# Performance work log

Measured on AMD Instinct MI355X. Metric: run time of the kernel, lower is better.

The kernel has to match this reference:

```python
import jax, jax.numpy as jnp
import numpy as np

B, T, D_MODEL, D_HEAD = 8, 2048, 1024, 64


def setup_inputs() -> dict:
    key = jax.random.key(0)
    kx, kq, kk, kv = jax.random.split(key, 4)
    s = 1.0 / np.sqrt(D_MODEL)
    return {
        "x": jax.random.normal(kx, (B, T, D_MODEL), dtype=jnp.float32),
        "W_Q": jax.random.normal(kq, (D_MODEL, D_HEAD), dtype=jnp.float32) * s,
        "W_K": jax.random.normal(kk, (D_MODEL, D_HEAD), dtype=jnp.float32) * s,
        "W_V": jax.random.normal(kv, (D_MODEL, D_HEAD), dtype=jnp.float32) * s,
    }


def reference(x, W_Q, W_K, W_V):
    # x: [B, T, d_model]; projections -> [B, T, d_head]
    q = jnp.einsum("btd,dh->bth", x, W_Q)
    k = jnp.einsum("btd,dh->bth", x, W_K)
    v = jnp.einsum("btd,dh->bth", x, W_V)
    d_head = W_Q.shape[-1]
    scale = 1.0 / jnp.sqrt(jnp.asarray(d_head, dtype=x.dtype))
    # scores: [B, T, T], causal mask (lower-triangular kept)
    scores = jnp.einsum("bqh,bkh->bqk", q, k) * scale
    T_ = x.shape[1]
    causal = jnp.tril(jnp.ones((T_, T_), dtype=bool))
    scores = jnp.where(causal[None, :, :], scores, jnp.asarray(-jnp.inf, dtype=x.dtype))
    a = jax.nn.softmax(scores, axis=-1)
    # dropout omitted (eval mode / identity)
    out = jnp.einsum("bqk,bkh->bqh", a, v)
    return out
```

## Files before the change

kernel.cpp:

```cpp
#include <hip/hip_runtime.h>

#define TT   2048
#define DM   1024
#define DH   64
#define NB   8
#define BK   128
#define KST  72

typedef __attribute__((ext_vector_type(4))) float          f32x4;
typedef __attribute__((ext_vector_type(4))) int            i32x4;
typedef __attribute__((ext_vector_type(4))) unsigned short u16x4;
typedef __attribute__((ext_vector_type(8))) short          s16x8;

__device__ __forceinline__ unsigned short f2bf(float f) {
  unsigned int u = __float_as_uint(f);
  u += 0x7fffu + ((u >> 16) & 1u);
  return (unsigned short)(u >> 16);
}

#define MFMA(acc, a, b) \
  (acc) = __builtin_amdgcn_mfma_f32_16x16x32_bf16((a), (b), (acc), 0, 0, 0)

__device__ __forceinline__ void gload_lds16(const void* g, void* l) {
  __builtin_amdgcn_global_load_lds(
      (const __attribute__((address_space(1))) void*)g,
      (__attribute__((address_space(3))) void*)l, 16, 0, 0);
}

#define WS_WT    0u
#define WS_QK    393216u
#define WS_VT    4587520u
#define WS_OP    6684672u
#define WS_ML    24510464u

__global__ __launch_bounds__(256) void pack_w_kernel(
    const float* __restrict__ wq, const float* __restrict__ wk,
    const float* __restrict__ wv, unsigned short* __restrict__ wt) {
  int idx = blockIdx.x * 256 + threadIdx.x;
  if (idx >= 192 * DM) return;
  int n = idx >> 10;
  int k = idx & (DM - 1);
  const float* src = (n < 64) ? wq : ((n < 128) ? wk : wv);
  wt[(size_t)n * DM + k] = f2bf(src[(size_t)k * DH + (n & 63)]);
}

__global__ __launch_bounds__(256) void qkv_gemm_kernel(
    const float* __restrict__ x, const unsigned short* __restrict__ wt,
    unsigned short* __restrict__ qkvqk, unsigned short* __restrict__ vt) {
  __shared__ __align__(16) float          a_lds[32 * BK];
  __shared__ __align__(16) unsigned short b_lds[192 * BK];

  const int tid  = threadIdx.x;
  const int lane = tid & 63;
  const int w    = tid >> 6;
  const int ln   = lane & 15;
  const int quad = lane >> 4;
  const int mw   = w & 1;
  const int nw   = w >> 1;
  const int m0   = blockIdx.x * 32;
  const int n0   = nw * 96;
  const int lsw  = ln & 7;

  int agoff[4];
  #pragma unroll
  for (int i = 0; i < 4; ++i) {
    int s = i * 256 + w * 64 + lane;
    int m = s >> 5, cc = s & 31;
    agoff[i] = (m0 + m) * DM + ((cc ^ (m & 7)) << 2);
  }
  int bgoff[12];
  #pragma unroll
  for (int j = 0; j < 12; ++j) {
    int s = j * 256 + w * 64 + lane;
    int n = s >> 4, cc = s & 15;
    bgoff[j] = n * DM + ((cc ^ (n & 7)) << 3);
  }

  f32x4 acc[6];
  #pragma unroll
  for (int i = 0; i < 6; ++i) acc[i] = (f32x4){0.f, 0.f, 0.f, 0.f};
  union { s16x8 v; unsigned short h[8]; } ap;

  #pragma unroll
  for (int i = 0; i < 4; ++i)
    gload_lds16(x + agoff[i], (void*)(a_lds + (i * 256 + w * 64) * 4));
  #pragma unroll
  for (int j = 0; j < 12; ++j)
    gload_lds16(wt + bgoff[j], (void*)(b_lds + (j * 256 + w * 64) * 8));

  for (int k0 = 0; k0 < DM; k0 += BK) {
    __syncthreads();
    #pragma unroll
    for (int ks = 0; ks < BK; ks += 32) {
      const int m  = mw * 16 + ln;
      const int c0 = (ks >> 2) + 2 * quad;
      f32x4 v0 = *(const f32x4*)&a_lds[m * BK + ((c0 ^ lsw) << 2)];
      f32x4 v1 = *(const f32x4*)&a_lds[m * BK + (((c0 + 1) ^ lsw) << 2)];
      #pragma unroll
      for (int j = 0; j < 4; ++j) { ap.h[j] = f2bf(v0[j]); ap.h[4 + j] = f2bf(v1[j]); }
      s16x8 af = ap.v;
      const int cb = (ks >> 3) + quad;
      #pragma unroll
      for (int nt = 0; nt < 6; ++nt) {
        int n = n0 + nt * 16 + ln;
        s16x8 bf = *(const s16x8*)&b_lds[n * BK + ((cb ^ lsw) << 3)];
        MFMA(acc[nt], af, bf);
      }
    }
    __syncthreads();
    if (k0 + BK < DM) {
      const int kn = k0 + BK;
      #pragma unroll
      for (int i = 0; i < 4; ++i)
        gload_lds16(x + agoff[i] + kn, (void*)(a_lds + (i * 256 + w * 64) * 4));
      #pragma unroll
      for (int j = 0; j < 12; ++j)
        gload_lds16(wt + bgoff[j] + kn, (void*)(b_lds + (j * 256 + w * 64) * 8));
    }
  }

  const float QS = 0.18033688011112042f;
  const int mm0 = m0 + mw * 16;
  const int bz  = mm0 >> 11;
  const int tb  = (mm0 & 2047) + quad * 4;
  #pragma unroll
  for (int nt = 0; nt < 6; ++nt) {
    const int ncol = n0 + nt * 16 + ln;
    if (ncol < 128) {
      const float sc = (ncol < 64) ? QS : 1.0f;
      #pragma unroll
      for (int r = 0; r < 4; ++r) {
        int row = mm0 + quad * 4 + r;
        qkvqk[(size_t)row * 128 + ncol] = f2bf(acc[nt][r] * sc);
      }
    } else {
      int d = ncol - 128;
      u16x4 h;
      #pragma unroll
      for (int r = 0; r < 4; ++r) h[r] = f2bf(acc[nt][r]);
      *(u16x4*)(vt + ((size_t)bz * 64 + d) * TT + tb) = h;
    }
  }
}

__global__ __launch_bounds__(512) void attn_part_kernel(
    const unsigned short* __restrict__ qkvqk, const unsigned short* __restrict__ vt,
    unsigned short* __restrict__ opart, float* __restrict__ ml) {
  const int Ctab[16] = {0,1,3,6,10,15,21,28,36,45,55,66,78,91,105,120};
  const int f  = blockIdx.x;
  const int bz = f / 136;
  const int rw = f - bz * 136;
  int s = 0;
  #pragma unroll
  for (int t = 1; t < 16; ++t) if (rw >= Ctab[t]) s = t;
  const int c = rw - Ctab[s];

  __shared__ __align__(16) unsigned short k_lds[2][64 * 64];
  __shared__ __align__(16) unsigned short v_lds[2][64 * 64];
  __shared__ __align__(16) unsigned short p_lds[2 * 64 * KST];

  const int tid  = threadIdx.x;
  const int w    = tid >> 6;
  const int grp  = w >> 2;
  const int wq   = w & 3;
  const int lane = tid & 63;
  const int ln   = lane & 15;
  const int quad = lane >> 4;
  const int lsw  = ln & 7;
  const int bb   = bz * TT;
  const int kbase = c * 128;
  const int qt   = 2 * s + grp;

  const int slot = w * 64 + lane;
  const int srow = slot >> 3, scc = slot & 7;
  const unsigned short* kgp =
      qkvqk + (size_t)(bb + kbase + srow) * 128 + 64 + ((scc ^ (srow & 7)) << 3);
  const unsigned short* vgp =
      vt + ((size_t)bz * 64 + srow) * TT + kbase + ((scc ^ (srow & 7)) << 3);

  const unsigned short* qrow = qkvqk + (size_t)(bb + qt * 64 + wq * 16 + ln) * 128;
  const s16x8 qf0 = *(const s16x8*)(qrow + quad * 8);
  const s16x8 qf1 = *(const s16x8*)(qrow + 32 + quad * 8);

  s16x8 ones;
  #pragma unroll
  for (int j = 0; j < 8; ++j) ones[j] = (short)0x3F80;

  f32x4 acc_o[4], acc_l;
  #pragma unroll
  for (int i = 0; i < 4; ++i) acc_o[i] = (f32x4){0.f, 0.f, 0.f, 0.f};
  acc_l = (f32x4){0.f, 0.f, 0.f, 0.f};

  unsigned short* pb = p_lds + grp * 64 * KST;
  const int qg = qt * 64 + wq * 16 + quad * 4;

  gload_lds16(kgp, (void*)(k_lds[0] + (w * 64) * 8));
  gload_lds16(vgp, (void*)(v_lds[0] + (w * 64) * 8));
  __syncthreads();
  gload_lds16(kgp + 64 * 128, (void*)(k_lds[1] + (w * 64) * 8));
  gload_lds16(vgp + 64,       (void*)(v_lds[1] + (w * 64) * 8));

  #pragma unroll
  for (int ct = 0; ct < 2; ++ct) {
    const unsigned short* kb = k_lds[ct];
    const unsigned short* vb = v_lds[ct];
    const int ktg = c * 2 + ct;
    if (ktg <= qt) {
      const bool diag = (ktg == qt);
      f32x4 acc_s[4];
      #pragma unroll
      for (int i = 0; i < 4; ++i) acc_s[i] = (f32x4){0.f, 0.f, 0.f, 0.f};
      __builtin_amdgcn_s_setprio(1);
      #pragma unroll
      for (int ns = 0; ns < 4; ++ns) {
        const int krow = ns * 16 + ln;
        s16x8 kf0 = *(const s16x8*)&kb[krow * 64 + ((quad ^ lsw) << 3)];
        s16x8 kf1 = *(const s16x8*)&kb[krow * 64 + (((4 + quad) ^ lsw) << 3)];
        MFMA(acc_s[ns], qf0, kf0);
        MFMA(acc_s[ns], qf1, kf1);
      }
      __builtin_amdgcn_s_setprio(0);
      #pragma unroll
      for (int r = 0; r < 4; ++r) {
        const int qgr = qg + r;
        #pragma unroll
        for (int ns = 0; ns < 4; ++ns) {
          float sv = acc_s[ns][r];
          if (diag) {
            int kg = ktg * 64 + ns * 16 + ln;
            sv = (kg <= qgr) ? sv : -1e30f;
          }
          pb[(wq * 16 + quad * 4 + r) * KST + ns * 16 + ln] =
              f2bf(__builtin_amdgcn_exp2f(sv));
        }
      }
      __builtin_amdgcn_s_setprio(1);
      #pragma unroll
      for (int kk = 0; kk < 64; kk += 32) {
        s16x8 pf = *(const s16x8*)&pb[(wq * 16 + ln) * KST + kk + quad * 8];
        MFMA(acc_l, pf, ones);
        #pragma unroll
        for (int nt = 0; nt < 4; ++nt) {
          const int d  = nt * 16 + ln;
          const int sc = ((kk >> 3) + quad) ^ lsw;
          s16x8 vf = *(const s16x8*)&vb[d * 64 + sc * 8];
          MFMA(acc_o[nt], pf, vf);
        }
      }
      __builtin_amdgcn_s_setprio(0);
      asm volatile("" ::: "memory");
    }
    if (ct == 0) __syncthreads();
  }

  const int base = (qt & 1) ? (s + 1) * (s + 1) : s * (s + 1);
  const size_t slab = (size_t)bz * 272 + base + c;
  unsigned short* op = opart + slab * 4096;
  #pragma unroll
  for (int nt = 0; nt < 4; ++nt)
    #pragma unroll
    for (int r = 0; r < 4; ++r)
      op[(wq * 16 + quad * 4 + r) * 64 + nt * 16 + ln] = f2bf(acc_o[nt][r]);
  if (ln == 0) {
    float* lp = ml + slab * 64;
    #pragma unroll
    for (int r = 0; r < 4; ++r)
      lp[wq * 16 + quad * 4 + r] = acc_l[r];
  }
}

__global__ __launch_bounds__(256) void attn_combine_kernel(
    const unsigned short* __restrict__ opart, const float* __restrict__ ml,
    float* __restrict__ out) {
  const int qt = blockIdx.x;
  const int bz = blockIdx.y;
  const int g  = qt >> 1;
  const int nch = g + 1;
  const int base = (qt & 1) ? (g + 1) * (g + 1) : g * (g + 1);
  const size_t slab0 = (size_t)bz * 272 + base;

  const int tid = threadIdx.x;
  const int row = tid >> 2;
  const int ds  = (tid & 3) * 16;

  float L = 0.f;
  float acc[16];
  #pragma unroll
  for (int j = 0; j < 16; ++j) acc[j] = 0.f;
  #pragma unroll 4
  for (int ch = 0; ch < nch; ++ch) {
    L += ml[(slab0 + ch) * 64 + row];
    const unsigned short* op = opart + (slab0 + ch) * 4096 + row * 64 + ds;
    i32x4 v0 = *(const i32x4*)(op);
    i32x4 v1 = *(const i32x4*)(op + 8);
    #pragma unroll
    for (int j = 0; j < 4; ++j) {
      unsigned int u0 = (unsigned int)v0[j], u1 = (unsigned int)v1[j];
      acc[j * 2]         += __uint_as_float(u0 << 16);
      acc[j * 2 + 1]     += __uint_as_float(u0 & 0xffff0000u);
      acc[8 + j * 2]     += __uint_as_float(u1 << 16);
      acc[8 + j * 2 + 1] += __uint_as_float(u1 & 0xffff0000u);
    }
  }
  float inv = 1.0f / L;
  float* o = out + ((size_t)bz * TT + qt * 64 + row) * 64 + ds;
  #pragma unroll
  for (int j = 0; j < 16; ++j) o[j] = acc[j] * inv;
}

extern "C" void kernel_launch(void* const* d_in, const int* in_sizes, int n_in,
                              void* d_out, int out_size, void* d_ws, size_t ws_size,
                              hipStream_t stream) {
  const float* x  = (const float*)d_in[0];
  const float* wq = (const float*)d_in[1];
  const float* wk = (const float*)d_in[2];
  const float* wv = (const float*)d_in[3];
  float* out = (float*)d_out;

  char* ws = (char*)d_ws;
  unsigned short* wt    = (unsigned short*)(ws + WS_WT);
  unsigned short* qkvqk = (unsigned short*)(ws + WS_QK);
  unsigned short* vt    = (unsigned short*)(ws + WS_VT);
  unsigned short* opart = (unsigned short*)(ws + WS_OP);
  float*          ml    = (float*)(ws + WS_ML);

  pack_w_kernel<<<(192 * DM + 255) / 256, 256, 0, stream>>>(wq, wk, wv, wt);
  qkv_gemm_kernel<<<NB * TT / 32, 256, 0, stream>>>(x, wt, qkvqk, vt);
  attn_part_kernel<<<NB * 136, 512, 0, stream>>>(qkvqk, vt, opart, ml);
  attn_combine_kernel<<<dim3(32, NB), 256, 0, stream>>>(opart, ml, out);
}
```

Measured before the change: 131.2 us.

## Split attention blocks to one query tile each with swizzled P buffer

New measurement: 131.5 us. No clear change (+0.3%).

```diff
diff --git a/kernel.cpp b/kernel.cpp
--- a/kernel.cpp
+++ b/kernel.cpp
@@ -5,7 +5,6 @@
 #define DH   64
 #define NB   8
 #define BK   128
-#define KST  72
 
 typedef __attribute__((ext_vector_type(4))) float          f32x4;
 typedef __attribute__((ext_vector_type(4))) int            i32x4;
@@ -143,42 +142,37 @@
   }
 }
 
-__global__ __launch_bounds__(512) void attn_part_kernel(
+__global__ __launch_bounds__(256) void attn_part_kernel(
     const unsigned short* __restrict__ qkvqk, const unsigned short* __restrict__ vt,
     unsigned short* __restrict__ opart, float* __restrict__ ml) {
-  const int Ctab[16] = {0,1,3,6,10,15,21,28,36,45,55,66,78,91,105,120};
   const int f  = blockIdx.x;
-  const int bz = f / 136;
-  const int rw = f - bz * 136;
-  int s = 0;
-  #pragma unroll
-  for (int t = 1; t < 16; ++t) if (rw >= Ctab[t]) s = t;
-  const int c = rw - Ctab[s];
+  const int bz = f / 272;
+  const int rw = f - bz * 272;
+  int qt = 0;
+  #pragma unroll
+  for (int t = 1; t < 32; ++t) {
+    int tg = t >> 1;
+    int bs = (t & 1) ? (tg + 1) * (tg + 1) : tg * (tg + 1);
+    if (rw >= bs) qt = t;
+  }
+  const int g    = qt >> 1;
+  const int base = (qt & 1) ? (g + 1) * (g + 1) : g * (g + 1);
+  const int c    = rw - base;
 
   __shared__ __align__(16) unsigned short k_lds[2][64 * 64];
   __shared__ __align__(16) unsigned short v_lds[2][64 * 64];
-  __shared__ __align__(16) unsigned short p_lds[2 * 64 * KST];
+  __shared__ __align__(16) unsigned short p_lds[64 * 64];
 
   const int tid  = threadIdx.x;
   const int w    = tid >> 6;
-  const int grp  = w >> 2;
-  const int wq   = w & 3;
   const int lane = tid & 63;
   const int ln   = lane & 15;
   const int quad = lane >> 4;
   const int lsw  = ln & 7;
   const int bb   = bz * TT;
   const int kbase = c * 128;
-  const int qt   = 2 * s + grp;
-
-  const int slot = w * 64 + lane;
-  const int srow = slot >> 3, scc = slot & 7;
-  const unsigned short* kgp =
-      qkvqk + (size_t)(bb + kbase + srow) * 128 + 64 + ((scc ^ (srow & 7)) << 3);
-  const unsigned short* vgp =
-      vt + ((size_t)bz * 64 + srow) * TT + kbase + ((scc ^ (srow & 7)) << 3);
-
-  const unsigned short* qrow = qkvqk + (size_t)(bb + qt * 64 + wq * 16 + ln) * 128;
+
+  const unsigned short* qrow = qkvqk + (size_t)(bb + qt * 64 + w * 16 + ln) * 128;
   const s16x8 qf0 = *(const s16x8*)(qrow + quad * 8);
   const s16x8 qf1 = *(const s16x8*)(qrow + 32 + quad * 8);
 
@@ -191,14 +185,42 @@
   for (int i = 0; i < 4; ++i) acc_o[i] = (f32x4){0.f, 0.f, 0.f, 0.f};
   acc_l = (f32x4){0.f, 0.f, 0.f, 0.f};
 
-  unsigned short* pb = p_lds + grp * 64 * KST;
-  const int qg = qt * 64 + wq * 16 + quad * 4;
-
-  gload_lds16(kgp, (void*)(k_lds[0] + (w * 64) * 8));
-  gload_lds16(vgp, (void*)(v_lds[0] + (w * 64) * 8));
+  const int qg = qt * 64 + w * 16 + quad * 4;
+
+  #pragma unroll
+  for (int i = 0; i < 2; ++i) {
+    int bse = i * 256 + w * 64;
+    int slot = bse + lane;
+    int row = slot >> 3, cc = slot & 7;
+    gload_lds16(qkvqk + (size_t)(bb + kbase + row) * 128 + 64 + ((cc ^ (row & 7)) << 3),
+                (void*)(k_lds[0] + bse * 8));
+  }
+  #pragma unroll
+  for (int i = 0; i < 2; ++i) {
+    int bse = i * 256 + w * 64;
+    int slot = bse + lane;
+    int d = slot >> 3, cc = slot & 7;
+    gload_lds16(vt + ((size_t)bz * 64 + d) * TT + kbase + ((cc ^ (d & 7)) << 3),
+                (void*)(v_lds[0] + bse * 8));
+  }
   __syncthreads();
-  gload_lds16(kgp + 64 * 128, (void*)(k_lds[1] + (w * 64) * 8));
-  gload_lds16(vgp + 64,       (void*)(v_lds[1] + (w * 64) * 8));
+  #pragma unroll
+  for (int i = 0; i < 2; ++i) {
+    int bse = i * 256 + w * 64;
+    int slot = bse + lane;
+    int row = slot >> 3, cc = slot & 7;
+    gload_lds16(
+        qkvqk + (size_t)(bb + kbase + 64 + row) * 128 + 64 + ((cc ^ (row & 7)) << 3),
+        (void*)(k_lds[1] + bse * 8));
+  }
+  #pragma unroll
+  for (int i = 0; i < 2; ++i) {
+    int bse = i * 256 + w * 64;
+    int slot = bse + lane;
+    int d = slot >> 3, cc = slot & 7;
+    gload_lds16(vt + ((size_t)bz * 64 + d) * TT + kbase + 64 + ((cc ^ (d & 7)) << 3),
+                (void*)(v_lds[1] + bse * 8));
+  }
 
   #pragma unroll
   for (int ct = 0; ct < 2; ++ct) {
@@ -223,6 +245,7 @@
       #pragma unroll
       for (int r = 0; r < 4; ++r) {
         const int qgr = qg + r;
+        const int prow = w * 16 + quad * 4 + r;
         #pragma unroll
         for (int ns = 0; ns < 4; ++ns) {
           float sv = acc_s[ns][r];
@@ -230,14 +253,16 @@
             int kg = ktg * 64 + ns * 16 + ln;
             sv = (kg <= qgr) ? sv : -1e30f;
           }
-          pb[(wq * 16 + quad * 4 + r) * KST + ns * 16 + ln] =
+          p_lds[prow * 64 + ((((ns << 1) + (ln >> 3)) ^ (prow & 7)) << 3) + (ln & 7)] =
               f2bf(__builtin_amdgcn_exp2f(sv));
         }
       }
       __builtin_amdgcn_s_setprio(1);
       #pragma unroll
       for (int kk = 0; kk < 64; kk += 32) {
-        s16x8 pf = *(const s16x8*)&pb[(wq * 16 + ln) * KST + kk + quad * 8];
+        const int prw = w * 16 + ln;
+        s16x8 pf = *(const s16x8*)
+            &p_lds[prw * 64 + ((((kk >> 3) + quad) ^ (prw & 7)) << 3)];
         MFMA(acc_l, pf, ones);
         #pragma unroll
         for (int nt = 0; nt < 4; ++nt) {
@@ -253,19 +278,18 @@
     if (ct == 0) __syncthreads();
   }
 
-  const int base = (qt & 1) ? (s + 1) * (s + 1) : s * (s + 1);
   const size_t slab = (size_t)bz * 272 + base + c;
   unsigned short* op = opart + slab * 4096;
   #pragma unroll
   for (int nt = 0; nt < 4; ++nt)
     #pragma unroll
     for (int r = 0; r < 4; ++r)
-      op[(wq * 16 + quad * 4 + r) * 64 + nt * 16 + ln] = f2bf(acc_o[nt][r]);
+      op[(w * 16 + quad * 4 + r) * 64 + nt * 16 + ln] = f2bf(acc_o[nt][r]);
   if (ln == 0) {
     float* lp = ml + slab * 64;
     #pragma unroll
     for (int r = 0; r < 4; ++r)
-      lp[wq * 16 + quad * 4 + r] = acc_l[r];
+      lp[w * 16 + quad * 4 + r] = acc_l[r];
   }
 }
 
@@ -326,6 +350,6 @@
 
   pack_w_kernel<<<(192 * DM + 255) / 256, 256, 0, stream>>>(wq, wk, wv, wt);
   qkv_gemm_kernel<<<NB * TT / 32, 256, 0, stream>>>(x, wt, qkvqk, vt);
-  attn_part_kernel<<<NB * 136, 512, 0, stream>>>(qkvqk, vt, opart, ml);
+  attn_part_kernel<<<NB * 272, 256, 0, stream>>>(qkvqk, vt, opart, ml);
   attn_combine_kernel<<<dim3(32, NB), 256, 0, stream>>>(opart, ml, out);
 }
```
